# Performance work log

Hardware: AMD Instinct MI355X
Metric: run time of the kernel (lower is better)

## Reference

```python
import jax, jax.numpy as jnp
import numpy as np
import math

PI = math.pi
L = 6.0 * math.pi
EPS = 1e-5


def c19_activation(x, rho=4.0):
    scaled = x * (1.0 / PI)
    n = jnp.floor(scaled)
    t = scaled - n
    h = t * (1.0 - t)
    sgn = jnp.where(jnp.remainder(n, 2.0) < 1.0, 1.0, -1.0)
    core = PI * (sgn * h + rho * h * h)
    return jnp.where(x >= L, x - L, jnp.where(x <= -L, x + L, core))


def layer_norm(x, gamma, beta):
    mu = jnp.mean(x, axis=-1, keepdims=True)
    var = jnp.mean(jnp.square(x - mu), axis=-1, keepdims=True)
    return (x - mu) * jax.lax.rsqrt(var + EPS) * gamma + beta


def setup_inputs() -> dict:
    key = jax.random.key(0)
    ks = jax.random.split(key, 8)
    B, T, NB, D, DEPTH = 65536, 32, 8, 128, 4
    nl = DEPTH - 1  # 3 inner layers
    x = jax.random.normal(ks[0], (B, T, NB), dtype=jnp.float32)
    Wi = jax.random.normal(ks[1], (NB, D), dtype=jnp.float32) * 0.1   # input_proj (in, out)
    bi = jnp.zeros((D,), jnp.float32)
    Wo = jax.random.normal(ks[2], (D, NB), dtype=jnp.float32) * 0.1   # output_proj
    bo = jnp.zeros((NB,), jnp.float32)
    g_state = jnp.ones((D,), jnp.float32)
    b_state = jnp.zeros((D,), jnp.float32)
    Ws = jax.random.normal(ks[3], (nl, D, D), dtype=jnp.float32) * (1.0 / math.sqrt(D))
    bs = jnp.zeros((nl, D), jnp.float32)
    gs = jnp.ones((nl, D), jnp.float32)
    betas = jnp.zeros((nl, D), jnp.float32)
    return {"x": x, "Wi": Wi, "bi": bi, "Wo": Wo, "bo": bo,
            "g_state": g_state, "b_state": b_state,
            "Ws": Ws, "bs": bs, "gs": gs, "betas": betas}


def reference(x, Wi, bi, Wo, bo, g_state, b_state, Ws, bs, gs, betas):
    B, T, _ = x.shape
    D = Wi.shape[1]
    nl = Ws.shape[0]

    def step(h, xt):  # h: [B,D], xt: [B,NB]
        inp = xt @ Wi + bi
        state = 0.618 * layer_norm(h, g_state, b_state) + 0.382 * inp
        for i in range(nl):  # fixed small depth loop
            state = state + c19_activation(layer_norm(state, gs[i], betas[i]) @ Ws[i] + bs[i])
        out = state @ Wo + bo
        return state, out

    h0 = jnp.zeros((B, D), dtype=x.dtype)
    _, outs = jax.lax.scan(step, h0, jnp.swapaxes(x, 0, 1))  # outs: [T,B,NB]
    return jnp.swapaxes(outs, 0, 1)  # [B,T,NB]
```

## Files before the change

kernel.cpp:

```cpp
#include <hip/hip_runtime.h>
#include <math.h>

#define BDIM 512
#define BR   64
#define D    128
#define SPD  130
#define WSP  130
#define SWOP 12
#define TT   32
#define NB   8
#define NL   3

typedef double v4d __attribute__((ext_vector_type(4)));

__device__ __forceinline__ double c19_act_d(double x) {
    const double PI_D = 3.14159265358979323846;
    const double L6   = 6.0 * PI_D;
    double scaled = x * (1.0 / PI_D);
    double n = floor(scaled);
    double t = scaled - n;
    double h = t * (1.0 - t);
    double halfn = n * 0.5;
    double fr = halfn - floor(halfn);
    double sgn = (fr < 0.25) ? 1.0 : -1.0;
    double core = PI_D * (sgn * h + 4.0 * h * h);
    double r = core;
    r = (x <= -L6) ? (x + L6) : r;
    r = (x >=  L6) ? (x - L6) : r;
    return r;
}

__global__ void miniphi_prep(const float* __restrict__ Ws, const float* __restrict__ gs,
                             double* __restrict__ wp) {
    int idx = blockIdx.x * 256 + threadIdx.x;
    wp[idx] = (double)gs[idx >> 7] * (double)Ws[idx];
}

__global__ __launch_bounds__(BDIM) void miniphi_kernel(
    const float* __restrict__ x,  const float* __restrict__ Wi, const float* __restrict__ bi,
    const float* __restrict__ Wo, const float* __restrict__ bo,
    const float* __restrict__ g_state, const float* __restrict__ b_state,
    const float* __restrict__ Ws, const float* __restrict__ bs,
    const float* __restrict__ gs, const float* __restrict__ betas,
    const double* __restrict__ wp,
    float* __restrict__ out)
{
    __shared__ double sState[BR][SPD];
    __shared__ double sWq[2][32][WSP];
    __shared__ float  sWi[NB][D];
    __shared__ float  sWo[D][SWOP];
    __shared__ float  sBi[D], sGst[D], sBst[D];
    __shared__ double sGsD[NL][D];
    __shared__ double sGW[NL][D];
    __shared__ double sBWbs[NL][D];
    __shared__ double sRstd[BR], sMu2[BR];
    __shared__ float  sBo[NB];
    __shared__ int    sPR[64][4], sPC[64][4];
    __shared__ int    sFlag;

    const int tid  = threadIdx.x;
    const int lane = tid & 63;
    const int wv   = tid >> 6;

    for (int i = tid; i < NB * D; i += BDIM) sWi[i >> 7][i & 127] = Wi[i];
    for (int i = tid; i < D * NB; i += BDIM) sWo[i >> 3][i & 7] = Wo[i];
    for (int i = tid; i < D; i += BDIM) { sBi[i] = bi[i]; sGst[i] = g_state[i]; sBst[i] = b_state[i]; }
    for (int i = tid; i < NL * D; i += BDIM) sGsD[i >> 7][i & 127] = (double)gs[i];
    if (tid < NB) sBo[tid] = bo[tid];
    for (int i = tid; i < BR * D; i += BDIM) sState[i >> 7][i & 127] = 0.0;
    if (tid < NL * D) {
        int ly = tid >> 7, c = tid & 127;
        const float* wl = Ws + (size_t)ly * D * D;
        double gw = 0.0, bw = 0.0;
        for (int k = 0; k < D; ++k) {
            double w = (double)wl[k * D + c];
            gw = fma((double)gs[ly * D + k], w, gw);
            bw = fma((double)betas[ly * D + k], w, bw);
        }
        sGW[ly][c] = gw;
        sBWbs[ly][c] = bw + (double)bs[ly * D + c];
    }

    if (wv == 0) {
        const int lm = lane & 15, lk = lane >> 4;
        v4d z = {0.0, 0.0, 0.0, 0.0};
        v4d p1 = __builtin_amdgcn_mfma_f64_16x16x4f64((double)lm, 1.0, z, 0, 0, 0);
        v4d p2 = __builtin_amdgcn_mfma_f64_16x16x4f64(1.0, (double)lm, z, 0, 0, 0);
        double pk = (double)(1 << lk);
        v4d p3 = __builtin_amdgcn_mfma_f64_16x16x4f64(pk, pk, z, 0, 0, 0);
        v4d p4 = __builtin_amdgcn_mfma_f64_16x16x4f64(1.0 + 0x1p-30, 1.0, z, 0, 0, 0);
        double pa5 = (lk == 0) ? 1.0 : 0x1p-52;
        v4d p5 = __builtin_amdgcn_mfma_f64_16x16x4f64(pa5, 1.0, z, 0, 0, 0);
        bool ok = true;
        #pragma unroll
        for (int i = 0; i < 4; ++i) {
            double v = p1[i]; int r = (int)(v * 0.25 + 0.5);
            ok = ok && (v == 4.0 * (double)r) && (r >= 0) && (r < 16);
            sPR[lane][i] = r;
            double w = p2[i]; int c2 = (int)(w * 0.25 + 0.5);
            ok = ok && (w == 4.0 * (double)c2) && (c2 >= 0) && (c2 < 16);
            sPC[lane][i] = c2;
            ok = ok && (p3[i] == 85.0);
            ok = ok && (p4[i] == 4.0 + 0x1p-28);
            ok = ok && (p5[i] == 1.0 + 3.0 * 0x1p-52);
        }
        unsigned long long bal = __ballot(ok ? 1 : 0);
        if (lane == 0) sFlag = (bal == 0xFFFFFFFFFFFFFFFFull) ? 1 : 0;
    }
    __syncthreads();

    const int useMfma = sFlag;
    int pr[4], pc[4];
    #pragma unroll
    for (int i = 0; i < 4; ++i) { pr[i] = sPR[lane][i]; pc[i] = sPC[lane][i]; }

    const int rLN = tid >> 3;
    const int sL  = tid & 7;
    const int lm  = lane & 15, lk = lane >> 4;
    const int n0  = wv * 16;
    const size_t rowg = (size_t)blockIdx.x * BR;

    #define STAGE_Q(LY, Q, QB)                                                      \
      { if (wp) {                                                                   \
          const double* src = wp + (((size_t)(LY) * D + (Q) * 32) * D);             \
          _Pragma("unroll")                                                         \
          for (int i_ = 0; i_ < 4; ++i_) {                                          \
              int kr_ = wv * 4 + i_;                                                \
              const double* g_ = src + (size_t)kr_ * D + lane * 2;                  \
              __builtin_amdgcn_global_load_lds(                                     \
                  (const __attribute__((address_space(1))) void*)g_,                \
                  (__attribute__((address_space(3))) void*)&sWq[QB][kr_][0],        \
                  16, 0, 0);                                                        \
          }                                                                         \
        } else {                                                                    \
          const float* src = Ws + (((size_t)(LY) * D + (Q) * 32) * D);              \
          const double* gl = &sGsD[LY][(Q) * 32];                                   \
          _Pragma("unroll")                                                         \
          for (int i_ = 0; i_ < 4; ++i_) {                                          \
              int kr_ = wv * 4 + i_;                                                \
              float2 w_ = *(const float2*)(src + (size_t)kr_ * D + lane * 2);       \
              double g_ = gl[kr_];                                                  \
              double2 o_; o_.x = g_ * (double)w_.x; o_.y = g_ * (double)w_.y;       \
              *(double2*)&sWq[QB][kr_][lane * 2] = o_;                              \
          }                                                                         \
        } }

    for (int t = 0; t < TT; ++t) {
        STAGE_Q(0, 0, 0)

        {
            const float* xp = x + (rowg + (size_t)rLN) * (TT * NB) + (size_t)t * NB;
            float4 xa = *(const float4*)(xp);
            float4 xb = *(const float4*)(xp + 4);
            double xv[8] = {(double)xa.x, (double)xa.y, (double)xa.z, (double)xa.w,
                            (double)xb.x, (double)xb.y, (double)xb.z, (double)xb.w};
            double v[16];
            #pragma unroll
            for (int j = 0; j < 16; ++j) v[j] = sState[rLN][sL + 8 * j];
            double sum = 0.0;
            #pragma unroll
            for (int j = 0; j < 16; ++j) sum += v[j];
            sum += __shfl_xor(sum, 1); sum += __shfl_xor(sum, 2); sum += __shfl_xor(sum, 4);
            double mu = sum * (1.0 / 128.0);
            double sq = 0.0;
            #pragma unroll
            for (int j = 0; j < 16; ++j) { double dd = v[j] - mu; sq += dd * dd; }
            sq += __shfl_xor(sq, 1); sq += __shfl_xor(sq, 2); sq += __shfl_xor(sq, 4);
            double rstd = 1.0 / sqrt(sq * (1.0 / 128.0) + 1e-5);
            #pragma unroll
            for (int j = 0; j < 16; ++j) {
                int c = sL + 8 * j;
                double inp = (double)sBi[c];
                #pragma unroll
                for (int k = 0; k < 8; ++k)
                    inp = fma(xv[k], (double)sWi[k][c], inp);
                double ln = (v[j] - mu) * rstd * (double)sGst[c] + (double)sBst[c];
                sState[rLN][c] = 0.618 * ln + 0.382 * inp;
            }
        }

        for (int ly = 0; ly < NL; ++ly) {
            {
                double v[16];
                #pragma unroll
                for (int j = 0; j < 16; ++j) v[j] = sState[rLN][sL + 8 * j];
                double sum = 0.0;
                #pragma unroll
                for (int j = 0; j < 16; ++j) sum += v[j];
                sum += __shfl_xor(sum, 1); sum += __shfl_xor(sum, 2); sum += __shfl_xor(sum, 4);
                double mu = sum * (1.0 / 128.0);
                double sq = 0.0;
                #pragma unroll
                for (int j = 0; j < 16; ++j) { double dd = v[j] - mu; sq += dd * dd; }
                sq += __shfl_xor(sq, 1); sq += __shfl_xor(sq, 2); sq += __shfl_xor(sq, 4);
                double rstd = 1.0 / sqrt(sq * (1.0 / 128.0) + 1e-5);
                if (sL == 0) { sRstd[rLN] = rstd; sMu2[rLN] = mu * rstd; }
            }
            __syncthreads();

            v4d acc0 = {0,0,0,0}, acc1 = {0,0,0,0}, acc2 = {0,0,0,0}, acc3 = {0,0,0,0};
            double accv[4][2];
            #pragma unroll
            for (int r = 0; r < 4; ++r) { accv[r][0] = 0.0; accv[r][1] = 0.0; }

            #pragma unroll
            for (int q = 0; q < 4; ++q) {
                const int qb = q & 1, qk = q * 32;
                if (q < 3) { STAGE_Q(ly, q + 1, (q + 1) & 1) }

                if (useMfma) {
                    #pragma unroll
                    for (int k0 = 0; k0 < 32; k0 += 4) {
                        double b  = sWq[qb][k0 + lk][n0 + lm];
                        double a0 = sState[lm     ][qk + k0 + lk];
                        double a1 = sState[lm + 16][qk + k0 + lk];
                        double a2 = sState[lm + 32][qk + k0 + lk];
                        double a3 = sState[lm + 48][qk + k0 + lk];
                        acc0 = __builtin_amdgcn_mfma_f64_16x16x4f64(a0, b, acc0, 0, 0, 0);
                        acc1 = __builtin_amdgcn_mfma_f64_16x16x4f64(a1, b, acc1, 0, 0, 0);
                        acc2 = __builtin_amdgcn_mfma_f64_16x16x4f64(a2, b, acc2, 0, 0, 0);
                        acc3 = __builtin_amdgcn_mfma_f64_16x16x4f64(a3, b, acc3, 0, 0, 0);
                    }
                } else {
                    const int r0v = wv * 8;
                    #pragma unroll 4
                    for (int kk = 0; kk < 32; kk += 2) {
                        int kg = qk + kk;
                        double b00 = sWq[qb][kk][lane],     b01 = sWq[qb][kk][lane + 64];
                        double b10 = sWq[qb][kk + 1][lane], b11 = sWq[qb][kk + 1][lane + 64];
                        #pragma unroll
                        for (int r = 0; r < 4; ++r) {
                            double2 a = *(const double2*)&sState[r0v + 2 * r + (lane >> 6)][kg];
                            accv[r][0] = fma(a.y, b10, fma(a.x, b00, accv[r][0]));
                            accv[r][1] = fma(a.y, b11, fma(a.x, b01, accv[r][1]));
                        }
                    }
                }
                __syncthreads();
            }

            if (useMfma) {
                #pragma unroll
                for (int i = 0; i < 4; ++i) {
                    int col = n0 + pc[i];
                    double gwc = sGW[ly][col], bwc = sBWbs[ly][col];
                    int R0 = pr[i];
                    double y0 = fma(sRstd[R0],      acc0[i], fma(-sMu2[R0],      gwc, bwc));
                    double y1 = fma(sRstd[R0 + 16], acc1[i], fma(-sMu2[R0 + 16], gwc, bwc));
                    double y2 = fma(sRstd[R0 + 32], acc2[i], fma(-sMu2[R0 + 32], gwc, bwc));
                    double y3 = fma(sRstd[R0 + 48], acc3[i], fma(-sMu2[R0 + 48], gwc, bwc));
                    sState[R0][col]      += c19_act_d(y0);
                    sState[R0 + 16][col] += c19_act_d(y1);
                    sState[R0 + 32][col] += c19_act_d(y2);
                    sState[R0 + 48][col] += c19_act_d(y3);
                }
            } else {
                const int r0v = wv * 8;
                double gwc0 = sGW[ly][lane],   gwc1 = sGW[ly][lane + 64];
                double bwc0 = sBWbs[ly][lane], bwc1 = sBWbs[ly][lane + 64];
                #pragma unroll
                for (int r = 0; r < 4; ++r) {
                    int R = r0v + 2 * r;
                    double rs = sRstd[R], m2 = sMu2[R];
                    double y0 = fma(rs, accv[r][0], fma(-m2, gwc0, bwc0));
                    double y1 = fma(rs, accv[r][1], fma(-m2, gwc1, bwc1));
                    sState[R][lane]      += c19_act_d(y0);
                    sState[R][lane + 64] += c19_act_d(y1);
                }
            }
            __syncthreads();

            if (ly + 1 < NL) { STAGE_Q(ly + 1, 0, 0) }
        }

        {
            double accj[8];
            #pragma unroll
            for (int j = 0; j < 8; ++j) accj[j] = 0.0;
            #pragma unroll
            for (int u = 0; u < 16; ++u) {
                int k = sL + 8 * u;
                double s = sState[rLN][k];
                float4 w0 = *(const float4*)&sWo[k][0];
                float4 w1 = *(const float4*)&sWo[k][4];
                accj[0] = fma(s, (double)w0.x, accj[0]);
                accj[1] = fma(s, (double)w0.y, accj[1]);
                accj[2] = fma(s, (double)w0.z, accj[2]);
                accj[3] = fma(s, (double)w0.w, accj[3]);
                accj[4] = fma(s, (double)w1.x, accj[4]);
                accj[5] = fma(s, (double)w1.y, accj[5]);
                accj[6] = fma(s, (double)w1.z, accj[6]);
                accj[7] = fma(s, (double)w1.w, accj[7]);
            }
            #pragma unroll
            for (int j = 0; j < 8; ++j) {
                accj[j] += __shfl_xor(accj[j], 1);
                accj[j] += __shfl_xor(accj[j], 2);
                accj[j] += __shfl_xor(accj[j], 4);
            }
            double o = accj[0];
            #pragma unroll
            for (int j = 1; j < 8; ++j) o = (sL == j) ? accj[j] : o;
            out[((rowg + (size_t)rLN) * TT + (size_t)t) * NB + sL] =
                (float)(o + (double)sBo[sL]);
        }
    }
    #undef STAGE_Q
}

extern "C" void kernel_launch(void* const* d_in, const int* in_sizes, int n_in,
                              void* d_out, int out_size, void* d_ws, size_t ws_size,
                              hipStream_t stream) {
    const float* x       = (const float*)d_in[0];
    const float* Wi      = (const float*)d_in[1];
    const float* bi      = (const float*)d_in[2];
    const float* Wo      = (const float*)d_in[3];
    const float* bo      = (const float*)d_in[4];
    const float* g_state = (const float*)d_in[5];
    const float* b_state = (const float*)d_in[6];
    const float* Ws      = (const float*)d_in[7];
    const float* bs      = (const float*)d_in[8];
    const float* gs      = (const float*)d_in[9];
    const float* betas   = (const float*)d_in[10];
    float* out = (float*)d_out;

    const size_t wp_bytes = (size_t)NL * D * D * sizeof(double);
    double* wp = (ws_size >= wp_bytes) ? (double*)d_ws : nullptr;
    if (wp) {
        dim3 pgrid(NL * D * D / 256), pblock(256);
        hipLaunchKernelGGL(miniphi_prep, pgrid, pblock, 0, stream, Ws, gs, wp);
    }

    const int B = in_sizes[0] / (TT * NB);
    dim3 grid(B / BR), block(BDIM);
    hipLaunchKernelGGL(miniphi_kernel, grid, block, 0, stream,
                       x, Wi, bi, Wo, bo, g_state, b_state, Ws, bs, gs, betas, wp, out);
}
```

Baseline: 5.283 ms.

## Overlap layer-norm statistics with first GEMM quarter and prefetch next layer weights earlier

Unrolls the four K-quarters of each inner-layer GEMM into explicit stage-and-compute steps. The per-row mean/rstd reduction now runs after the first quarter's MFMAs, and the sync that used to sit between them is removed. The first weight quarter of the next layer, or of layer 0 for the next timestep, is staged while the last quarter is still being multiplied. This hides weight-load latency and drops one barrier per layer, at the cost of an extra barrier after the input projection. It also reworks the non-MFMA fallback so each wave covers all eight of its rows.

```diff
diff --git a/kernel.cpp b/kernel.cpp
--- a/kernel.cpp
+++ b/kernel.cpp
@@ -118,6 +118,7 @@
     const int sL  = tid & 7;
     const int lm  = lane & 15, lk = lane >> 4;
     const int n0  = wv * 16;
+    const int r0v = wv * 8;
     const size_t rowg = (size_t)blockIdx.x * BR;
 
     #define STAGE_Q(LY, Q, QB)                                                      \
@@ -145,9 +146,38 @@
           }                                                                         \
         } }
 
+    #define GEMM_Q(QB, QK)                                                          \
+      if (useMfma) {                                                                \
+          _Pragma("unroll")                                                         \
+          for (int k0 = 0; k0 < 32; k0 += 4) {                                      \
+              double b  = sWq[QB][k0 + lk][n0 + lm];                                \
+              double a0 = sState[lm     ][(QK) + k0 + lk];                          \
+              double a1 = sState[lm + 16][(QK) + k0 + lk];                          \
+              double a2 = sState[lm + 32][(QK) + k0 + lk];                          \
+              double a3 = sState[lm + 48][(QK) + k0 + lk];                          \
+              acc0 = __builtin_amdgcn_mfma_f64_16x16x4f64(a0, b, acc0, 0, 0, 0);    \
+              acc1 = __builtin_amdgcn_mfma_f64_16x16x4f64(a1, b, acc1, 0, 0, 0);    \
+              acc2 = __builtin_amdgcn_mfma_f64_16x16x4f64(a2, b, acc2, 0, 0, 0);    \
+              acc3 = __builtin_amdgcn_mfma_f64_16x16x4f64(a3, b, acc3, 0, 0, 0);    \
+          }                                                                         \
+      } else {                                                                      \
+          _Pragma("unroll 4")                                                       \
+          for (int kk = 0; kk < 32; kk += 2) {                                      \
+              int kg = (QK) + kk;                                                   \
+              double b00 = sWq[QB][kk][lane],     b01 = sWq[QB][kk][lane + 64];     \
+              double b10 = sWq[QB][kk + 1][lane], b11 = sWq[QB][kk + 1][lane + 64]; \
+              _Pragma("unroll")                                                     \
+              for (int r = 0; r < 8; ++r) {                                         \
+                  double2 a = *(const double2*)&sState[r0v + r][kg];                \
+                  accv[r][0] = fma(a.y, b10, fma(a.x, b00, accv[r][0]));            \
+                  accv[r][1] = fma(a.y, b11, fma(a.x, b01, accv[r][1]));            \
+              }                                                                     \
+          }                                                                         \
+      }
+
+    STAGE_Q(0, 0, 0)
+
     for (int t = 0; t < TT; ++t) {
-        STAGE_Q(0, 0, 0)
-
         {
             const float* xp = x + (rowg + (size_t)rLN) * (TT * NB) + (size_t)t * NB;
             float4 xa = *(const float4*)(xp);
@@ -178,66 +208,42 @@
                 sState[rLN][c] = 0.618 * ln + 0.382 * inp;
             }
         }
+        __syncthreads();
 
         for (int ly = 0; ly < NL; ++ly) {
+            v4d acc0 = {0,0,0,0}, acc1 = {0,0,0,0}, acc2 = {0,0,0,0}, acc3 = {0,0,0,0};
+            double accv[8][2];
+            #pragma unroll
+            for (int r = 0; r < 8; ++r) { accv[r][0] = 0.0; accv[r][1] = 0.0; }
+
+            STAGE_Q(ly, 1, 1)
+            GEMM_Q(0, 0)
             {
-                double v[16];
-                #pragma unroll
-                for (int j = 0; j < 16; ++j) v[j] = sState[rLN][sL + 8 * j];
                 double sum = 0.0;
                 #pragma unroll
-                for (int j = 0; j < 16; ++j) sum += v[j];
+                for (int j = 0; j < 16; ++j) sum += sState[rLN][sL + 8 * j];
                 sum += __shfl_xor(sum, 1); sum += __shfl_xor(sum, 2); sum += __shfl_xor(sum, 4);
                 double mu = sum * (1.0 / 128.0);
                 double sq = 0.0;
                 #pragma unroll
-                for (int j = 0; j < 16; ++j) { double dd = v[j] - mu; sq += dd * dd; }
+                for (int j = 0; j < 16; ++j) { double dd = sState[rLN][sL + 8 * j] - mu; sq += dd * dd; }
                 sq += __shfl_xor(sq, 1); sq += __shfl_xor(sq, 2); sq += __shfl_xor(sq, 4);
                 double rstd = 1.0 / sqrt(sq * (1.0 / 128.0) + 1e-5);
                 if (sL == 0) { sRstd[rLN] = rstd; sMu2[rLN] = mu * rstd; }
             }
             __syncthreads();
 
-            v4d acc0 = {0,0,0,0}, acc1 = {0,0,0,0}, acc2 = {0,0,0,0}, acc3 = {0,0,0,0};
-            double accv[4][2];
-            #pragma unroll
-            for (int r = 0; r < 4; ++r) { accv[r][0] = 0.0; accv[r][1] = 0.0; }
-
-            #pragma unroll
-            for (int q = 0; q < 4; ++q) {
-                const int qb = q & 1, qk = q * 32;
-                if (q < 3) { STAGE_Q(ly, q + 1, (q + 1) & 1) }
-
-                if (useMfma) {
-                    #pragma unroll
-                    for (int k0 = 0; k0 < 32; k0 += 4) {
-                        double b  = sWq[qb][k0 + lk][n0 + lm];
-                        double a0 = sState[lm     ][qk + k0 + lk];
-                        double a1 = sState[lm + 16][qk + k0 + lk];
-                        double a2 = sState[lm + 32][qk + k0 + lk];
-                        double a3 = sState[lm + 48][qk + k0 + lk];
-                        acc0 = __builtin_amdgcn_mfma_f64_16x16x4f64(a0, b, acc0, 0, 0, 0);
-                        acc1 = __builtin_amdgcn_mfma_f64_16x16x4f64(a1, b, acc1, 0, 0, 0);
-                        acc2 = __builtin_amdgcn_mfma_f64_16x16x4f64(a2, b, acc2, 0, 0, 0);
-                        acc3 = __builtin_amdgcn_mfma_f64_16x16x4f64(a3, b, acc3, 0, 0, 0);
-                    }
-                } else {
-                    const int r0v = wv * 8;
-                    #pragma unroll 4
-                    for (int kk = 0; kk < 32; kk += 2) {
-                        int kg = qk + kk;
-                        double b00 = sWq[qb][kk][lane],     b01 = sWq[qb][kk][lane + 64];
-                        double b10 = sWq[qb][kk + 1][lane], b11 = sWq[qb][kk + 1][lane + 64];
-                        #pragma unroll
-                        for (int r = 0; r < 4; ++r) {
-                            double2 a = *(const double2*)&sState[r0v + 2 * r + (lane >> 6)][kg];
-                            accv[r][0] = fma(a.y, b10, fma(a.x, b00, accv[r][0]));
-                            accv[r][1] = fma(a.y, b11, fma(a.x, b01, accv[r][1]));
-                        }
-                    }
-                }
-                __syncthreads();
-            }
+            STAGE_Q(ly, 2, 0)
+            GEMM_Q(1, 32)
+            __syncthreads();
+
+            STAGE_Q(ly, 3, 1)
+            GEMM_Q(0, 64)
+            __syncthreads();
+
+            if (ly + 1 < NL) { STAGE_Q(ly + 1, 0, 0) } else { STAGE_Q(0, 0, 0) }
+            GEMM_Q(1, 96)
+            __syncthreads();
 
             if (useMfma) {
                 #pragma unroll
@@ -255,12 +261,11 @@
                     sState[R0 + 48][col] += c19_act_d(y3);
                 }
             } else {
-                const int r0v = wv * 8;
                 double gwc0 = sGW[ly][lane],   gwc1 = sGW[ly][lane + 64];
                 double bwc0 = sBWbs[ly][lane], bwc1 = sBWbs[ly][lane + 64];
                 #pragma unroll
-                for (int r = 0; r < 4; ++r) {
-                    int R = r0v + 2 * r;
+                for (int r = 0; r < 8; ++r) {
+                    int R = r0v + r;
                     double rs = sRstd[R], m2 = sMu2[R];
                     double y0 = fma(rs, accv[r][0], fma(-m2, gwc0, bwc0));
                     double y1 = fma(rs, accv[r][1], fma(-m2, gwc1, bwc1));
@@ -269,8 +274,6 @@
                 }
             }
             __syncthreads();
-
-            if (ly + 1 < NL) { STAGE_Q(ly + 1, 0, 0) }
         }
 
         {
@@ -305,6 +308,7 @@
                 (float)(o + (double)sBo[sL]);
         }
     }
+    #undef GEMM_Q
     #undef STAGE_Q
 }
 
```

New measurement: 5.208 ms. About the same (-1.4%).
